# Kernel optimization log

Measured on AMD Instinct MI355X. Metric: run time of the kernel, lower is better.

Reference implementation:

```python
import jax, jax.numpy as jnp
import numpy as np

D_MODEL = 1024
N_HEADS = 16
D_HEAD = D_MODEL // N_HEADS


def setup_inputs() -> dict:
    key = jax.random.key(0)
    ks = jax.random.split(key, 5)
    scale = 1.0 / np.sqrt(D_MODEL)
    return {
        "x": jax.random.normal(ks[0], (2, 2048, D_MODEL), dtype=jnp.float32),
        "W_q": jax.random.normal(ks[1], (D_MODEL, D_MODEL), dtype=jnp.float32) * scale,
        "W_k": jax.random.normal(ks[2], (D_MODEL, D_MODEL), dtype=jnp.float32) * scale,
        "W_v": jax.random.normal(ks[3], (D_MODEL, D_MODEL), dtype=jnp.float32) * scale,
        "W_o": jax.random.normal(ks[4], (D_MODEL, D_MODEL), dtype=jnp.float32) * scale,
    }


def reference(x, W_q, W_k, W_v, W_o):
    B, S, _ = x.shape
    # nn.Linear computes x @ W.T; weights stored [out, in]
    def proj(W):
        y = jnp.einsum("bsd,ed->bse", x, W)
        return y.reshape(B, S, N_HEADS, D_HEAD).transpose(0, 2, 1, 3)  # [B,H,S,Dh]

    q, k, v = proj(W_q), proj(W_k), proj(W_v)
    scores = jnp.einsum("bhqd,bhkd->bhqk", q, k) / jnp.sqrt(jnp.float32(D_HEAD))
    causal = jnp.triu(jnp.ones((S, S), dtype=bool), k=1)
    scores = jnp.where(causal, -jnp.inf, scores)
    attn = jax.nn.softmax(scores, axis=-1)
    out = jnp.einsum("bhqk,bhkd->bhqd", attn, v)  # [B,H,S,Dh]
    out = out.transpose(0, 2, 1, 3).reshape(B, S, D_MODEL)
    return jnp.einsum("bsd,ed->bse", out, W_o)
```

## Files before the change

### kernel.cpp

```cpp
#include <hip/hip_runtime.h>


#define DMODEL 1024
#define NHEADS 16
#define DHEAD  64
#define SEQ    2048
#define BATCH  2
#define MROWS  (BATCH * SEQ)

typedef __bf16 bf16x8 __attribute__((ext_vector_type(8)));
typedef __bf16 bf16x4 __attribute__((ext_vector_type(4)));
typedef float  f32x4  __attribute__((ext_vector_type(4)));

__device__ __forceinline__ f32x4 mfma16(bf16x8 a, bf16x8 b, f32x4 c) {
    return __builtin_amdgcn_mfma_f32_16x16x32_bf16(a, b, c, 0, 0, 0);
}

__device__ __forceinline__ bf16x8 ld8(const float* p) {
    const f32x4 a0 = *(const f32x4*)p;
    const f32x4 a1 = *(const f32x4*)(p + 4);
    bf16x8 v;
    v[0] = (__bf16)a0[0]; v[1] = (__bf16)a0[1];
    v[2] = (__bf16)a0[2]; v[3] = (__bf16)a0[3];
    v[4] = (__bf16)a1[0]; v[5] = (__bf16)a1[1];
    v[6] = (__bf16)a1[2]; v[7] = (__bf16)a1[3];
    return v;
}

__device__ __forceinline__ void gll16(const __bf16* g, __bf16* l) {
    __builtin_amdgcn_global_load_lds(
        (const __attribute__((address_space(1))) void*)g,
        (__attribute__((address_space(3))) void*)l,
        16, 0, 0);
}

__global__ __launch_bounds__(256) void cvt_kernel(const float* __restrict__ x,
                                                  const float* __restrict__ Wq,
                                                  const float* __restrict__ Wk,
                                                  const float* __restrict__ Wv,
                                                  const float* __restrict__ Wo,
                                                  __bf16* __restrict__ xb,
                                                  __bf16* __restrict__ wcat) {
    const int c = blockIdx.x * 256 + threadIdx.x;
    if (c < 524288) {
        *(bf16x8*)(xb + (size_t)c * 8) = ld8(x + (size_t)c * 8);
    } else {
        const int i = c - 524288;
        const int w = i >> 17;
        const int j = i & 131071;
        const float* src = (w == 0) ? Wq : (w == 1) ? Wk : (w == 2) ? Wv : Wo;
        *(bf16x8*)(wcat + (size_t)w * DMODEL * DMODEL + (size_t)j * 8) =
            ld8(src + (size_t)j * 8);
    }
}

template <typename TC, int MREP, int NREP>
__device__ __forceinline__ void gemm_bb_body(const __bf16* __restrict__ A,
                                             const __bf16* __restrict__ W,
                                             TC* __restrict__ C,
                                             __bf16* __restrict__ VT,
                                             bool vt, int m0, int bn0, int cn0,
                                             float scale) {
    constexpr int K  = DMODEL;
    constexpr int TM = MREP * 32;
    constexpr int TN = NREP * 32;
    __shared__ __align__(16) __bf16 As[2][TM][32];
    __shared__ __align__(16) __bf16 Bs[2][TN][32];

    const int tid  = threadIdx.x;
    const int lane = tid & 63;
    const int wave = tid >> 6;
    const int quad = lane >> 4;
    const int l16  = lane & 15;
    const int wm   = wave & 1;
    const int wn   = wave >> 1;

    const int srow = lane >> 2;
    const int scol = (lane & 3) * 8;

    const __bf16* ap = A + (size_t)(m0 + srow) * K + scol;
    const __bf16* bp = W + (size_t)(bn0 + srow) * K + scol;

    f32x4 acc[MREP][NREP] = {};

#pragma unroll
    for (int j = 0; j < MREP / 2; ++j) {
        const int r = wave * (MREP * 8) + j * 16;
        gll16(ap + (size_t)r * K, &As[0][r][0]);
    }
#pragma unroll
    for (int j = 0; j < NREP / 2; ++j) {
        const int r = wave * (NREP * 8) + j * 16;
        gll16(bp + (size_t)r * K, &Bs[0][r][0]);
    }
    __syncthreads();

    int cur = 0;
    for (int k0 = 0; k0 < K; k0 += 32) {
        if (k0 + 32 < K) {
            const int kn = k0 + 32;
#pragma unroll
            for (int j = 0; j < MREP / 2; ++j) {
                const int r = wave * (MREP * 8) + j * 16;
                gll16(ap + (size_t)r * K + kn, &As[cur ^ 1][r][0]);
            }
#pragma unroll
            for (int j = 0; j < NREP / 2; ++j) {
                const int r = wave * (NREP * 8) + j * 16;
                gll16(bp + (size_t)r * K + kn, &Bs[cur ^ 1][r][0]);
            }
        }

        bf16x8 af[MREP], bfr[NREP];
#pragma unroll
        for (int i = 0; i < MREP; ++i)
            af[i] = *(const bf16x8*)(&As[cur][wm * (MREP * 16) + i * 16 + l16][quad * 8]);
#pragma unroll
        for (int j = 0; j < NREP; ++j)
            bfr[j] = *(const bf16x8*)(&Bs[cur][wn * (NREP * 16) + j * 16 + l16][quad * 8]);
#pragma unroll
        for (int mi = 0; mi < MREP; ++mi)
#pragma unroll
            for (int ni = 0; ni < NREP; ++ni)
                acc[mi][ni] = mfma16(af[mi], bfr[ni], acc[mi][ni]);

        __syncthreads();
        cur ^= 1;
    }

    if (!vt) {
#pragma unroll
        for (int mi = 0; mi < MREP; ++mi)
#pragma unroll
            for (int ni = 0; ni < NREP; ++ni)
#pragma unroll
                for (int r = 0; r < 4; ++r) {
                    int row = m0 + wm * (MREP * 16) + mi * 16 + quad * 4 + r;
                    int col = cn0 + wn * (NREP * 16) + ni * 16 + l16;
                    C[(size_t)row * DMODEL + col] = (TC)(acc[mi][ni][r] * scale);
                }
    } else {
#pragma unroll
        for (int mi = 0; mi < MREP; ++mi)
#pragma unroll
            for (int ni = 0; ni < NREP; ++ni) {
                const int m  = m0 + wm * (MREP * 16) + mi * 16 + quad * 4;
                const int hd = cn0 + wn * (NREP * 16) + ni * 16 + l16;
                bf16x4 v4;
#pragma unroll
                for (int r = 0; r < 4; ++r) v4[r] = (__bf16)acc[mi][ni][r];
                *(bf16x4*)(VT + (size_t)hd * MROWS + m) = v4;
            }
    }
}

#define QSCALE 0.1803368801111204f

__global__ __launch_bounds__(256) void qkv_kernel(const __bf16* __restrict__ X,
                                                  const __bf16* __restrict__ wcat,
                                                  __bf16* __restrict__ Q,
                                                  __bf16* __restrict__ K,
                                                  __bf16* __restrict__ VT) {
    const int bn0 = blockIdx.x * 128;
    const int z   = bn0 >> 10;
    const int cn0 = bn0 - (z << 10);
    __bf16* Y = (z == 0) ? Q : K;
    const float scale = (z == 0) ? QSCALE : 1.0f;
    gemm_bb_body<__bf16, 4, 4>(X, wcat, Y, VT, z == 2,
                               blockIdx.y * 128, bn0, cn0, scale);
}

__global__ __launch_bounds__(256) void out_gemm_kernel(const __bf16* __restrict__ A,
                                                       const __bf16* __restrict__ W,
                                                       float* __restrict__ C) {
    gemm_bb_body<float, 2, 4>(A, W, C, nullptr, false,
                              blockIdx.y * 64, blockIdx.x * 128, blockIdx.x * 128,
                              1.0f);
}

__global__ __launch_bounds__(256) void attn_kernel(const __bf16* __restrict__ Q,
                                                   const __bf16* __restrict__ Kg,
                                                   const __bf16* __restrict__ VTg,
                                                   __bf16* __restrict__ O) {
    const int bh  = blockIdx.x;
    const int y   = blockIdx.y;
    const int ya  = y >> 3, yr = y & 7;
    const int qt2 = (ya == 0) ? (31 - yr)
                  : (ya == 1) ? (16 + yr)
                  : (ya == 2) ? (15 - yr)
                  :             yr;
    const int b = bh >> 4, h = bh & 15;
    const size_t base = (size_t)b * SEQ * DMODEL + (size_t)h * DHEAD;

    const int tid  = threadIdx.x;
    const int lane = tid & 63;
    const int wave = tid >> 6;
    const int quad = lane >> 4;
    const int l16  = lane & 15;

    __shared__ __align__(16) __bf16 Ks[2][64][64];
    __shared__ __align__(16) __bf16 Vs[2][64][64];
    __shared__ __align__(16) __bf16 Ps[4][2][16][40];

    const int sr = lane >> 3;
    const int sc = ((lane & 7) ^ sr) * 8;

    const int qrow = qt2 * 64 + wave * 16 + l16;

    const bf16x8 qf0 = *(const bf16x8*)(Q + base + (size_t)qrow * DMODEL + quad * 8);
    const bf16x8 qf1 = *(const bf16x8*)(Q + base + (size_t)qrow * DMODEL + 32 + quad * 8);

    const __bf16* kp = Kg + base + (size_t)(wave * 16 + sr) * DMODEL + sc;
    const __bf16* vp = VTg + (size_t)(h * 64 + wave * 16 + sr) * MROWS
                           + (size_t)b * SEQ + sc;

    bf16x8 ones;
#pragma unroll
    for (int i = 0; i < 8; ++i) ones[i] = (__bf16)1.0f;

    f32x4 oacc[4] = {};
    f32x4 lacc = {};

    const int ntiles = qt2 + 1;
    const int gsw = (l16 & 7);

    gll16(kp, &Ks[0][wave * 16][0]);
    gll16(kp + (size_t)8 * DMODEL, &Ks[0][wave * 16 + 8][0]);
    gll16(vp, &Vs[0][wave * 16][0]);
    gll16(vp + (size_t)8 * MROWS, &Vs[0][wave * 16 + 8][0]);
    __syncthreads();

    int cur = 0;
    for (int kt = 0; kt < ntiles; ++kt) {
        const int k0 = kt * 64;

        if (kt + 1 < ntiles) {
            const __bf16* kpt = kp + (size_t)(k0 + 64) * DMODEL;
            const __bf16* vpt = vp + (k0 + 64);
            gll16(kpt, &Ks[cur ^ 1][wave * 16][0]);
            gll16(kpt + (size_t)8 * DMODEL, &Ks[cur ^ 1][wave * 16 + 8][0]);
            gll16(vpt, &Vs[cur ^ 1][wave * 16][0]);
            gll16(vpt + (size_t)8 * MROWS, &Vs[cur ^ 1][wave * 16 + 8][0]);
        }

        const bool diag = (kt == ntiles - 1);

        f32x4 s[4];
#pragma unroll
        for (int g = 0; g < 4; ++g) {
            const bf16x8 kfa = *(const bf16x8*)(&Ks[cur][g * 16 + l16][(quad ^ gsw) * 8]);
            const bf16x8 kfb = *(const bf16x8*)(&Ks[cur][g * 16 + l16][((quad + 4) ^ gsw) * 8]);
            f32x4 t = {};
            t = mfma16(kfa, qf0, t);
            t = mfma16(kfb, qf1, t);
            s[g] = t;
        }

        bf16x4 w4[4];
        if (!diag) {
#pragma unroll
            for (int g = 0; g < 4; ++g)
#pragma unroll
                for (int r = 0; r < 4; ++r)
                    w4[g][r] = (__bf16)exp2f(s[g][r]);
        } else {
#pragma unroll
            for (int g = 0; g < 4; ++g)
#pragma unroll
                for (int r = 0; r < 4; ++r) {
                    const int kk = k0 + g * 16 + quad * 4 + r;
                    w4[g][r] = (kk <= qrow) ? (__bf16)exp2f(s[g][r]) : (__bf16)0.f;
                }
        }

#pragma unroll
        for (int g = 0; g < 4; ++g)
            *(bf16x4*)(&Ps[wave][g >> 1][l16][(g & 1) * 16 + quad * 4]) = w4[g];

        const bf16x8 pf0 = *(const bf16x8*)(&Ps[wave][0][l16][quad * 8]);
        const bf16x8 pf1 = *(const bf16x8*)(&Ps[wave][1][l16][quad * 8]);
        lacc = mfma16(ones, pf0, lacc);
        lacc = mfma16(ones, pf1, lacc);
#pragma unroll
        for (int f = 0; f < 4; ++f) {
            const bf16x8 vfa = *(const bf16x8*)(&Vs[cur][f * 16 + l16][(quad ^ gsw) * 8]);
            const bf16x8 vfb = *(const bf16x8*)(&Vs[cur][f * 16 + l16][((quad + 4) ^ gsw) * 8]);
            f32x4 t = oacc[f];
            t = mfma16(vfa, pf0, t);
            t = mfma16(vfb, pf1, t);
            oacc[f] = t;
        }

        __syncthreads();
        cur ^= 1;
    }

    const float l_i = lacc[0];
    const float inv = (l_i > 0.f) ? (1.f / l_i) : 0.f;
#pragma unroll
    for (int f = 0; f < 4; ++f) {
        bf16x4 o;
#pragma unroll
        for (int r = 0; r < 4; ++r) o[r] = (__bf16)(oacc[f][r] * inv);
        *(bf16x4*)(O + base + (size_t)qrow * DMODEL + f * 16 + quad * 4) = o;
    }
}

extern "C" void kernel_launch(void* const* d_in, const int* in_sizes, int n_in,
                              void* d_out, int out_size, void* d_ws, size_t ws_size,
                              hipStream_t stream) {
    const float* x  = (const float*)d_in[0];
    const float* Wq = (const float*)d_in[1];
    const float* Wk = (const float*)d_in[2];
    const float* Wv = (const float*)d_in[3];
    const float* Wo = (const float*)d_in[4];
    float* out = (float*)d_out;

    const size_t tm = (size_t)MROWS * DMODEL;
    const size_t tw = (size_t)DMODEL * DMODEL;
    __bf16* Q    = (__bf16*)d_ws;
    __bf16* K    = Q + tm;
    __bf16* VT   = K + tm;
    __bf16* xb   = VT + tm;
    __bf16* wcat = xb + tm;

    cvt_kernel<<<4096, 256, 0, stream>>>(x, Wq, Wk, Wv, Wo, xb, wcat);

    dim3 g1(3072 / 128, MROWS / 128);
    qkv_kernel<<<g1, 256, 0, stream>>>(xb, wcat, Q, K, VT);

    dim3 g2(BATCH * NHEADS, SEQ / 64);
    attn_kernel<<<g2, 256, 0, stream>>>(Q, K, VT, Q);

    dim3 g3(DMODEL / 128, MROWS / 64);
    out_gemm_kernel<<<g3, 256, 0, stream>>>(Q, wcat + 3 * tw, out);
}
```

Measured before the change: 183.2 us.

## Triple-buffer GEMM LDS loads with explicit vmcnt waits and raw barriers

```diff
diff --git a/kernel.cpp b/kernel.cpp
--- a/kernel.cpp
+++ b/kernel.cpp
@@ -14,6 +14,11 @@
 
 __device__ __forceinline__ f32x4 mfma16(bf16x8 a, bf16x8 b, f32x4 c) {
     return __builtin_amdgcn_mfma_f32_16x16x32_bf16(a, b, c, 0, 0, 0);
+}
+
+template <int N>
+__device__ __forceinline__ void waitcnt_vm() {
+    asm volatile("s_waitcnt vmcnt(%0)" :: "i"(N) : "memory");
 }
 
 __device__ __forceinline__ bf16x8 ld8(const float* p) {
@@ -64,8 +69,9 @@
     constexpr int K  = DMODEL;
     constexpr int TM = MREP * 32;
     constexpr int TN = NREP * 32;
-    __shared__ __align__(16) __bf16 As[2][TM][32];
-    __shared__ __align__(16) __bf16 Bs[2][TN][32];
+    constexpr int L  = MREP / 2 + NREP / 2;
+    __shared__ __align__(16) __bf16 As[3][TM][32];
+    __shared__ __align__(16) __bf16 Bs[3][TN][32];
 
     const int tid  = threadIdx.x;
     const int lane = tid & 63;
@@ -83,33 +89,35 @@
 
     f32x4 acc[MREP][NREP] = {};
 
-#pragma unroll
-    for (int j = 0; j < MREP / 2; ++j) {
-        const int r = wave * (MREP * 8) + j * 16;
-        gll16(ap + (size_t)r * K, &As[0][r][0]);
-    }
-#pragma unroll
-    for (int j = 0; j < NREP / 2; ++j) {
-        const int r = wave * (NREP * 8) + j * 16;
-        gll16(bp + (size_t)r * K, &Bs[0][r][0]);
-    }
-    __syncthreads();
+    auto stage = [&](int kn, int buf) {
+#pragma unroll
+        for (int j = 0; j < MREP / 2; ++j) {
+            const int r = wave * (MREP * 8) + j * 16;
+            gll16(ap + (size_t)r * K + kn, &As[buf][r][0]);
+        }
+#pragma unroll
+        for (int j = 0; j < NREP / 2; ++j) {
+            const int r = wave * (NREP * 8) + j * 16;
+            gll16(bp + (size_t)r * K + kn, &Bs[buf][r][0]);
+        }
+    };
+
+    stage(0, 0);
+    stage(32, 1);
 
     int cur = 0;
     for (int k0 = 0; k0 < K; k0 += 32) {
-        if (k0 + 32 < K) {
-            const int kn = k0 + 32;
-#pragma unroll
-            for (int j = 0; j < MREP / 2; ++j) {
-                const int r = wave * (MREP * 8) + j * 16;
-                gll16(ap + (size_t)r * K + kn, &As[cur ^ 1][r][0]);
-            }
-#pragma unroll
-            for (int j = 0; j < NREP / 2; ++j) {
-                const int r = wave * (NREP * 8) + j * 16;
-                gll16(bp + (size_t)r * K + kn, &Bs[cur ^ 1][r][0]);
-            }
-        }
+        if (k0 + 64 < K) {
+            int b2 = cur + 2; if (b2 >= 3) b2 -= 3;
+            stage(k0 + 64, b2);
+            waitcnt_vm<2 * L>();
+        } else if (k0 + 32 < K) {
+            waitcnt_vm<L>();
+        } else {
+            waitcnt_vm<0>();
+        }
+        __builtin_amdgcn_s_barrier();
+        __builtin_amdgcn_sched_barrier(0);
 
         bf16x8 af[MREP], bfr[NREP];
 #pragma unroll
@@ -124,8 +132,10 @@
             for (int ni = 0; ni < NREP; ++ni)
                 acc[mi][ni] = mfma16(af[mi], bfr[ni], acc[mi][ni]);
 
-        __syncthreads();
-        cur ^= 1;
+        __builtin_amdgcn_sched_barrier(0);
+        __builtin_amdgcn_s_barrier();
+        int c1 = cur + 1; if (c1 >= 3) c1 -= 3;
+        cur = c1;
     }
 
     if (!vt) {
```

After: 177.6 us. 1.03x faster.
